# Optimization experiments

Measured on AMD Instinct MI355X. Metric: run time of the kernel, lower is better.

## Reference

```python
import jax, jax.numpy as jnp
import numpy as np

B, T, V, E, H = 128, 256, 50000, 256, 512
H2 = H // 2
NTAGS = 76
START_IDX, STOP_IDX = 74, 75
NEG = -10000.0


def setup_inputs() -> dict:
    key = jax.random.key(0)
    ks = jax.random.split(key, 16)
    input_ids = jax.random.randint(ks[0], (B, T), 0, V, dtype=jnp.int32)
    embed_table = jax.random.normal(ks[1], (V, E), dtype=jnp.float32) * 0.02
    s = 0.05
    Wih_f = jax.random.normal(ks[2], (4 * H2, E)) * s
    Whh_f = jax.random.normal(ks[3], (4 * H2, H2)) * s
    bih_f = jnp.zeros((4 * H2,), jnp.float32)
    bhh_f = jnp.zeros((4 * H2,), jnp.float32)
    Wih_b = jax.random.normal(ks[4], (4 * H2, E)) * s
    Whh_b = jax.random.normal(ks[5], (4 * H2, H2)) * s
    bih_b = jnp.zeros((4 * H2,), jnp.float32)
    bhh_b = jnp.zeros((4 * H2,), jnp.float32)
    # init_hidden uses torch.randn each call -> random initial states
    h0 = jax.random.normal(ks[6], (2, B, H2), dtype=jnp.float32)
    c0 = jax.random.normal(ks[7], (2, B, H2), dtype=jnp.float32)
    W_out = jax.random.normal(ks[8], (NTAGS, H)) * s
    b_out = jnp.zeros((NTAGS,), jnp.float32)
    transitions = jax.random.normal(ks[9], (NTAGS, NTAGS), dtype=jnp.float32)
    transitions = transitions.at[START_IDX, :].set(NEG).at[:, STOP_IDX].set(NEG)
    return dict(input_ids=input_ids, embed_table=embed_table,
                Wih_f=Wih_f, Whh_f=Whh_f, bih_f=bih_f, bhh_f=bhh_f,
                Wih_b=Wih_b, Whh_b=Whh_b, bih_b=bih_b, bhh_b=bhh_b,
                h0=h0, c0=c0, W_out=W_out, b_out=b_out, transitions=transitions)


def _lstm(x, h0, c0, Wih, Whh, bih, bhh):
    # x: [B,T,E] -> outputs [B,T,H2]; PyTorch gate order i,f,g,o
    def step(carry, xt):
        h, c = carry
        gates = xt @ Wih.T + h @ Whh.T + (bih + bhh)  # [B,4*H2]
        i, f, g, o = jnp.split(gates, 4, axis=-1)
        c = jax.nn.sigmoid(f) * c + jax.nn.sigmoid(i) * jnp.tanh(g)
        h = jax.nn.sigmoid(o) * jnp.tanh(c)
        return (h, c), h
    _, hs = jax.lax.scan(step, (h0, c0), jnp.swapaxes(x, 0, 1))  # [T,B,H2]
    return jnp.swapaxes(hs, 0, 1)


def _viterbi(feats, transitions):
    # feats: [T,NTAGS]; transitions[next, prev]
    init = jnp.full((NTAGS,), NEG, feats.dtype).at[START_IDX].set(0.0)

    def step(fv, feat):
        scores = fv[None, :] + transitions          # [next, prev]
        bptr = jnp.argmax(scores, axis=1)           # [NTAGS]
        fv_new = jnp.max(scores, axis=1) + feat
        return fv_new, bptr

    fv, bptrs = jax.lax.scan(step, init, feats)     # bptrs: [T,NTAGS]
    terminal = fv + transitions[STOP_IDX]
    best = jnp.argmax(terminal)
    score = terminal[best]

    def back(tag, bptr):
        return bptr[tag], tag
    _, path = jax.lax.scan(back, best, bptrs, reverse=True)  # [T]
    return score, path


def reference(input_ids, embed_table, Wih_f, Whh_f, bih_f, bhh_f,
              Wih_b, Whh_b, bih_b, bhh_b, h0, c0, W_out, b_out, transitions):
    embeds = embed_table[input_ids]                              # [B,T,E]
    out_f = _lstm(embeds, h0[0], c0[0], Wih_f, Whh_f, bih_f, bhh_f)
    out_b = _lstm(embeds[:, ::-1], h0[1], c0[1], Wih_b, Whh_b, bih_b, bhh_b)[:, ::-1]
    lstm_out = jnp.concatenate([out_f, out_b], axis=-1)          # [B,T,H]
    feats = lstm_out @ W_out.T + b_out                           # [B,T,NTAGS]
    score, path = jax.vmap(_viterbi, in_axes=(0, None))(feats, transitions)
    return score, path
```

## Files before the change

### kernel.cpp

```cpp
#include <hip/hip_runtime.h>
#include <hip/hip_bf16.h>
#include <stdint.h>


#define T_      256
#define NT_     76
#define K3_     768
#define START_  74
#define STOP_   75
#define NEGV    (-10000.0f)

#define OFF_A3    ((size_t)0)
#define OFF_B3T   (OFF_A3    + (size_t)50331648)
#define OFF_XPROJ (OFF_B3T   + (size_t)3145728)
#define OFF_LSTM  (OFF_XPROJ + (size_t)67108864)
#define OFF_HBUF  (OFF_LSTM  + (size_t)67108864)
#define OFF_CBUF  (OFF_HBUF  + (size_t)524288)
#define OFF_CNT   (OFF_CBUF  + (size_t)262144)
#define OFF_FEATS OFF_A3

typedef __attribute__((ext_vector_type(8))) short short8;
typedef __attribute__((ext_vector_type(4))) float float4v;
typedef const __attribute__((address_space(1))) unsigned int gas_uint;
typedef __attribute__((address_space(3))) unsigned int las_uint;

__device__ __forceinline__ unsigned short f2bf(float x) {
    unsigned int u = __float_as_uint(x);
    u = (u + 0x7fffu + ((u >> 16) & 1u)) >> 16;
    return (unsigned short)u;
}
__device__ __forceinline__ float bf2f(unsigned short h) {
    return __uint_as_float(((unsigned int)h) << 16);
}
__device__ __forceinline__ void gl_lds16(const void* g, void* l) {
    __builtin_amdgcn_global_load_lds((gas_uint*)g, (las_uint*)l, 16, 0, 0);
}
__device__ __forceinline__ float4v llc_ld4(const float* p) {
    float4v r;
    asm volatile("global_load_dwordx4 %0, %1, off sc0 sc1" : "=v"(r) : "v"(p) : "memory");
    return r;
}
__device__ __forceinline__ void llc_st(float* p, float v) {
    asm volatile("global_store_dword %0, %1, off sc0 sc1" :: "v"(p), "v"(v) : "memory");
}
__device__ __forceinline__ void wait_vm0() { asm volatile("s_waitcnt vmcnt(0)" ::: "memory"); }

__global__ __launch_bounds__(64) void init_cnt(unsigned int* cnt) {
    if (threadIdx.x < 16) cnt[threadIdx.x * 64] = 0u;
}

__global__ __launch_bounds__(256) void build_a3(const int* __restrict__ ids,
                                                const float* __restrict__ emb,
                                                unsigned short* __restrict__ a3) {
    int m = blockIdx.x, k = threadIdx.x;
    int id = ids[m];
    float x = emb[(size_t)id * 256 + k];
    unsigned short hu = f2bf(x);
    unsigned short lu = f2bf(x - bf2f(hu));
    size_t base = (size_t)m * K3_;
    a3[base + k]       = hu;
    a3[base + 256 + k] = hu;
    a3[base + 512 + k] = lu;
}

__global__ __launch_bounds__(256) void build_b3t(const float* __restrict__ wf,
                                                 const float* __restrict__ wb,
                                                 unsigned short* __restrict__ b3t) {
    int n = blockIdx.x, k = threadIdx.x;
    const float* w = (n < 1024) ? wf : wb;
    int j = n & 1023;
    float x = w[(size_t)j * 256 + k];
    unsigned short hu = f2bf(x);
    unsigned short lu = f2bf(x - bf2f(hu));
    size_t base = (size_t)n * K3_;
    b3t[base + k]       = hu;
    b3t[base + 256 + k] = lu;
    b3t[base + 512 + k] = hu;
}

__global__ __launch_bounds__(256) void gemm_chunk(const unsigned short* __restrict__ A,
                                                  const unsigned short* __restrict__ Bt,
                                                  float* __restrict__ C, int t0) {
    __shared__ __align__(16) unsigned short As[128 * 64];
    __shared__ __align__(16) unsigned short Bs[128 * 64];
    int tid = threadIdx.x, bx = blockIdx.x;
    int d = bx >> 9, rem = bx & 511;
    int tm = rem >> 3, tn = rem & 7;
    int m0 = tm * 128, n0l = tn * 128;
    int tbase = d ? (192 - t0) : t0;
    int lane = tid & 63, wave = tid >> 6;
    int wm = (wave & 1) * 64, wn = (wave >> 1) * 64;
    int quad = lane >> 4, r16 = lane & 15;

    float4v acc[4][4];
#pragma unroll
    for (int i = 0; i < 4; i++)
#pragma unroll
        for (int j = 0; j < 4; j++) acc[i][j] = (float4v){0.f, 0.f, 0.f, 0.f};

    for (int kt = 0; kt < 12; ++kt) {
        int k0 = kt * 64;
#pragma unroll
        for (int i = 0; i < 4; ++i) {
            int c = i * 256 + tid;
            int row = c >> 3, col = c & 7;
            int rowm = m0 + row;
            int arow = (rowm >> 6) * 256 + tbase + (rowm & 63);
            int brow = d * 1024 + n0l + row;
            gl_lds16(A  + (size_t)arow * K3_ + k0 + col * 8, (unsigned short*)As + (size_t)c * 8);
            gl_lds16(Bt + (size_t)brow * K3_ + k0 + col * 8, (unsigned short*)Bs + (size_t)c * 8);
        }
        __syncthreads();
#pragma unroll
        for (int kk = 0; kk < 64; kk += 32) {
            short8 a[4], b[4];
#pragma unroll
            for (int i = 0; i < 4; i++) {
                a[i] = *(const short8*)&As[(wm + i * 16 + r16) * 64 + kk + quad * 8];
                b[i] = *(const short8*)&Bs[(wn + i * 16 + r16) * 64 + kk + quad * 8];
            }
#pragma unroll
            for (int i = 0; i < 4; i++)
#pragma unroll
                for (int j = 0; j < 4; j++)
                    acc[i][j] = __builtin_amdgcn_mfma_f32_16x16x32_bf16(a[i], b[j], acc[i][j], 0, 0, 0);
        }
        __syncthreads();
    }
#pragma unroll
    for (int i = 0; i < 4; i++)
#pragma unroll
        for (int j = 0; j < 4; j++)
#pragma unroll
            for (int r = 0; r < 4; r++) {
                int ml = wm + i * 16 + quad * 4 + r;
                int rowm = m0 + ml;
                int b = rowm >> 6, tl = rowm & 63;
                int n = n0l + wn + j * 16 + r16;
                C[(((size_t)(d * 128 + b)) * 64 + tl) * 1024 + n] = acc[i][j][r];
            }
}

#define HSTR 20

__global__ __launch_bounds__(256) void lstm_rec(
    const float* __restrict__ xproj,
    const float* __restrict__ whh_f, const float* __restrict__ whh_b,
    const float* __restrict__ bih_f, const float* __restrict__ bhh_f,
    const float* __restrict__ bih_b, const float* __restrict__ bhh_b,
    const float* __restrict__ h0,    const float* __restrict__ c0,
    float* __restrict__ lstm_out, float* hbuf, float* cbuf,
    unsigned char* cntbase, int t0) {

    int bx = blockIdx.x;
    int xcd = bx & 7, m8 = bx >> 3;
    int cid = xcd * 2 + (m8 >> 4);
    int s   = m8 & 15;
    int d   = cid & 1, g = cid >> 1;
    int tid = threadIdx.x;

    int q = tid >> 6, r = tid & 63;
    int rowB = (r >> 4) * 256 + s * 16 + (r & 15);
    const float* whh = d ? whh_b : whh_f;
    float4 w4[16];
    {
        const float4* wp = (const float4*)(whh + (size_t)rowB * 256 + q * 64);
#pragma unroll
        for (int i = 0; i < 16; i++) w4[i] = wp[i];
    }

    int b2 = tid >> 4, u2 = tid & 15;
    int ug2 = s * 16 + u2;
    int bg2 = g * 16 + b2;
    const float* bih = d ? bih_b : bih_f;
    const float* bhh = d ? bhh_b : bhh_f;
    float bias[4];
#pragma unroll
    for (int gg = 0; gg < 4; gg++) bias[gg] = bih[gg * 256 + ug2] + bhh[gg * 256 + ug2];
    size_t cidx = ((size_t)d * 128 + bg2) * 256 + ug2;
    float cst = (t0 == 0) ? c0[cidx] : cbuf[cidx];

    __shared__ __align__(16) float h_lds[256 * HSTR];
    __shared__ __align__(16) float red[4 * 64 * HSTR];

    unsigned int* mycnt = (unsigned int*)(cntbase + (size_t)cid * 256);
    const size_t HB_PAR = (size_t)16 * 4096;
    size_t hb_c = (size_t)cid * 4096;

    float xp[4];
    {
        int tloc0 = d ? 63 : 0;
        const float* xb = xproj + (((size_t)(d * 128 + bg2)) * 64 + tloc0) * 1024 + ug2;
#pragma unroll
        for (int gg = 0; gg < 4; gg++) xp[gg] = xb[gg * 256];
    }

    for (int tl = 0; tl < 64; ++tl) {
        int t = t0 + tl;
        int t_src = d ? (255 - t) : t;

        if (t == 0) {
#pragma unroll
            for (int b = 0; b < 16; b++)
                h_lds[tid * HSTR + b] = h0[((size_t)d * 128 + g * 16 + b) * 256 + tid];
        } else {
            const float* hsrc = hbuf + (size_t)(t & 1) * HB_PAR + hb_c + (size_t)tid * 16;
            float4v v0 = llc_ld4(hsrc);
            float4v v1 = llc_ld4(hsrc + 4);
            float4v v2 = llc_ld4(hsrc + 8);
            float4v v3 = llc_ld4(hsrc + 12);
            wait_vm0();
            float4v* dst = (float4v*)&h_lds[tid * HSTR];
            dst[0] = v0; dst[1] = v1; dst[2] = v2; dst[3] = v3;
        }
        __syncthreads();

        float acc[16];
#pragma unroll
        for (int b = 0; b < 16; b++) acc[b] = 0.f;
        const float* hq = h_lds + q * 64 * HSTR;
#pragma unroll
        for (int k4 = 0; k4 < 16; ++k4) {
            float4 wv = w4[k4];
#pragma unroll
            for (int kk = 0; kk < 4; ++kk) {
                float wx = (kk == 0) ? wv.x : (kk == 1) ? wv.y : (kk == 2) ? wv.z : wv.w;
                const float4* hv = (const float4*)(hq + (k4 * 4 + kk) * HSTR);
                float4 ha = hv[0], hb4 = hv[1], hc = hv[2], hd = hv[3];
                acc[0]  += wx * ha.x;  acc[1]  += wx * ha.y;  acc[2]  += wx * ha.z;  acc[3]  += wx * ha.w;
                acc[4]  += wx * hb4.x; acc[5]  += wx * hb4.y; acc[6]  += wx * hb4.z; acc[7]  += wx * hb4.w;
                acc[8]  += wx * hc.x;  acc[9]  += wx * hc.y;  acc[10] += wx * hc.z;  acc[11] += wx * hc.w;
                acc[12] += wx * hd.x;  acc[13] += wx * hd.y;  acc[14] += wx * hd.z;  acc[15] += wx * hd.w;
            }
        }
        {
            float4* rp = (float4*)&red[(q * 64 + r) * HSTR];
            rp[0] = make_float4(acc[0], acc[1], acc[2], acc[3]);
            rp[1] = make_float4(acc[4], acc[5], acc[6], acc[7]);
            rp[2] = make_float4(acc[8], acc[9], acc[10], acc[11]);
            rp[3] = make_float4(acc[12], acc[13], acc[14], acc[15]);
        }
        __syncthreads();

        float gate[4];
#pragma unroll
        for (int gg = 0; gg < 4; gg++) {
            int rr = gg * 16 + u2;
            gate[gg] = red[(0 * 64 + rr) * HSTR + b2] + red[(1 * 64 + rr) * HSTR + b2] +
                       red[(2 * 64 + rr) * HSTR + b2] + red[(3 * 64 + rr) * HSTR + b2] +
                       xp[gg] + bias[gg];
        }
        float iv = 1.f / (1.f + expf(-gate[0]));
        float fv = 1.f / (1.f + expf(-gate[1]));
        float gv = tanhf(gate[2]);
        float ov = 1.f / (1.f + expf(-gate[3]));
        cst = fv * cst + iv * gv;
        float hv = ov * tanhf(cst);

        llc_st(hbuf + (size_t)((t + 1) & 1) * HB_PAR + hb_c + (size_t)ug2 * 16 + b2, hv);
        lstm_out[((size_t)bg2 * 256 + t_src) * 512 + d * 256 + ug2] = hv;
        wait_vm0();

        {
            int tln  = (tl < 63) ? tl + 1 : 63;
            int tloc = d ? (63 - tln) : tln;
            const float* xb = xproj + (((size_t)(d * 128 + bg2)) * 64 + tloc) * 1024 + ug2;
#pragma unroll
            for (int gg = 0; gg < 4; gg++) xp[gg] = xb[gg * 256];
        }
        __builtin_amdgcn_s_barrier();

        if (t < 255) {
            if (tid == 0) {
                __hip_atomic_fetch_add(mycnt, 1u, __ATOMIC_RELAXED, __HIP_MEMORY_SCOPE_AGENT);
                unsigned tgt = 16u * (unsigned)(t + 1);
                while (__hip_atomic_load(mycnt, __ATOMIC_RELAXED, __HIP_MEMORY_SCOPE_AGENT) < tgt)
                    __builtin_amdgcn_s_sleep(1);
            }
            __builtin_amdgcn_s_barrier();
        }
    }
    cbuf[cidx] = cst;
}

__global__ __launch_bounds__(256) void out_proj(const float* __restrict__ lstm,
                                                const float* __restrict__ wout,
                                                const float* __restrict__ bout,
                                                float* __restrict__ feats) {
    __shared__ __align__(16) float hrow[16 * 512];
    int tid = threadIdx.x;
    size_t m0 = (size_t)blockIdx.x * 16;
    {
        const float4* src = (const float4*)(lstm + m0 * 512);
        float4* dst = (float4*)hrow;
        for (int i = tid; i < 2048; i += 256) dst[i] = src[i];
    }
    __syncthreads();
    int n = tid & 127, rh = tid >> 7;
    int nn = (n < NT_) ? n : 0;
    float acc[8];
#pragma unroll
    for (int rr = 0; rr < 8; rr++) acc[rr] = 0.f;
    const float* wrow = wout + (size_t)nn * 512;
    for (int k = 0; k < 512; k += 4) {
        float4 wv = *(const float4*)&wrow[k];
#pragma unroll
        for (int rr = 0; rr < 8; ++rr) {
            float4 hv = *(const float4*)&hrow[(rh * 8 + rr) * 512 + k];
            acc[rr] += wv.x * hv.x + wv.y * hv.y + wv.z * hv.z + wv.w * hv.w;
        }
    }
    if (n < NT_) {
        float bb = bout[n];
#pragma unroll
        for (int rr = 0; rr < 8; ++rr)
            feats[(m0 + rh * 8 + rr) * NT_ + n] = acc[rr] + bb;
    }
}

__global__ __launch_bounds__(128) void viterbi(const float* __restrict__ feats,
                                               const float* __restrict__ trans,
                                               float* __restrict__ out) {
    int b = blockIdx.x, tid = threadIdx.x;
    __shared__ float fvbuf[2][80];
    __shared__ float termbuf[80];
    __shared__ unsigned char bptr[256][NT_];

    float trr[NT_];
    if (tid < NT_) {
#pragma unroll
        for (int p = 0; p < NT_; p++) trr[p] = trans[tid * NT_ + p];
    }
    if (tid < 80) fvbuf[0][tid] = (tid == START_) ? 0.f : NEGV;
    __syncthreads();

    const float* fb = feats + (size_t)b * T_ * NT_;
    for (int t = 0; t < T_; ++t) {
        int par = t & 1;
        if (tid < NT_) {
            float feat = fb[t * NT_ + tid];
            const float* fv = fvbuf[par];
            float best = fv[0] + trr[0];
            int arg = 0;
#pragma unroll
            for (int p = 1; p < NT_; ++p) {
                float sc = fv[p] + trr[p];
                if (sc > best) { best = sc; arg = p; }
            }
            bptr[t][tid] = (unsigned char)arg;
            fvbuf[1 - par][tid] = best + feat;
        }
        __syncthreads();
    }
    if (tid < NT_) termbuf[tid] = fvbuf[0][tid] + trans[STOP_ * NT_ + tid];
    __syncthreads();
    if (tid == 0) {
        float best = termbuf[0];
        int arg = 0;
        for (int p = 1; p < NT_; ++p)
            if (termbuf[p] > best) { best = termbuf[p]; arg = p; }
        out[b] = best;
        int tag = arg;
        float* pout = out + 128 + (size_t)b * T_;
        for (int t = T_ - 1; t >= 0; --t) {
            pout[t] = (float)tag;
            tag = bptr[t][tag];
        }
    }
}

extern "C" void kernel_launch(void* const* d_in, const int* in_sizes, int n_in,
                              void* d_out, int out_size, void* d_ws, size_t ws_size,
                              hipStream_t stream) {
    const int*   ids   = (const int*)  d_in[0];
    const float* emb   = (const float*)d_in[1];
    const float* wih_f = (const float*)d_in[2];
    const float* whh_f = (const float*)d_in[3];
    const float* bih_f = (const float*)d_in[4];
    const float* bhh_f = (const float*)d_in[5];
    const float* wih_b = (const float*)d_in[6];
    const float* whh_b = (const float*)d_in[7];
    const float* bih_b = (const float*)d_in[8];
    const float* bhh_b = (const float*)d_in[9];
    const float* h0    = (const float*)d_in[10];
    const float* c0    = (const float*)d_in[11];
    const float* wout  = (const float*)d_in[12];
    const float* bout  = (const float*)d_in[13];
    const float* trans = (const float*)d_in[14];

    char* ws = (char*)d_ws;
    unsigned short* A3  = (unsigned short*)(ws + OFF_A3);
    unsigned short* B3T = (unsigned short*)(ws + OFF_B3T);
    float* XPROJ        = (float*)(ws + OFF_XPROJ);
    float* LSTM         = (float*)(ws + OFF_LSTM);
    float* HBUF         = (float*)(ws + OFF_HBUF);
    float* CBUF         = (float*)(ws + OFF_CBUF);
    unsigned char* CNT  = (unsigned char*)(ws + OFF_CNT);
    float* FEATS        = (float*)(ws + OFF_FEATS);

    init_cnt <<<1,     64,  0, stream>>>((unsigned int*)CNT);
    build_a3 <<<32768, 256, 0, stream>>>(ids, emb, A3);
    build_b3t<<<2048,  256, 0, stream>>>(wih_f, wih_b, B3T);
    for (int c = 0; c < 4; ++c) {
        gemm_chunk<<<1024, 256, 0, stream>>>(A3, B3T, XPROJ, c * 64);
        lstm_rec  <<<256,  256, 0, stream>>>(XPROJ, whh_f, whh_b, bih_f, bhh_f, bih_b, bhh_b,
                                             h0, c0, LSTM, HBUF, CBUF, CNT, c * 64);
    }
    out_proj<<<2048, 256, 0, stream>>>(LSTM, wout, bout, FEATS);
    viterbi <<<128,  128, 0, stream>>>(FEATS, trans, (float*)d_out);
}
```

Baseline: 2.099 ms.

## Replace atomic counter barrier with step-tagged h exchange in LSTM recurrence

Drops the per-step atomic counter spin barrier between cooperating blocks. Each hidden value is now stored as a 64-bit pair of value and step tag, and readers poll their h slice until every tag matches the current step. The lstm_out writes move to the reader side, and the xproj loads move to the start of each step. This removes the serial atomic and barrier round trips from the critical path, but the h buffer is larger and the polling loads repeat until the data is ready. The tag scheme depends on stale tags from earlier runs never matching the current step.

```diff
diff --git a/kernel.cpp b/kernel.cpp
--- a/kernel.cpp
+++ b/kernel.cpp
@@ -15,12 +15,13 @@
 #define OFF_XPROJ (OFF_B3T   + (size_t)3145728)
 #define OFF_LSTM  (OFF_XPROJ + (size_t)67108864)
 #define OFF_HBUF  (OFF_LSTM  + (size_t)67108864)
-#define OFF_CBUF  (OFF_HBUF  + (size_t)524288)
-#define OFF_CNT   (OFF_CBUF  + (size_t)262144)
+#define OFF_CBUF  (OFF_HBUF  + (size_t)2097152)
 #define OFF_FEATS OFF_A3
 
 typedef __attribute__((ext_vector_type(8))) short short8;
 typedef __attribute__((ext_vector_type(4))) float float4v;
+typedef __attribute__((ext_vector_type(4))) unsigned int uint4v;
+typedef __attribute__((ext_vector_type(2))) unsigned int uint2v;
 typedef const __attribute__((address_space(1))) unsigned int gas_uint;
 typedef __attribute__((address_space(3))) unsigned int las_uint;
 
@@ -35,18 +36,17 @@
 __device__ __forceinline__ void gl_lds16(const void* g, void* l) {
     __builtin_amdgcn_global_load_lds((gas_uint*)g, (las_uint*)l, 16, 0, 0);
 }
-__device__ __forceinline__ float4v llc_ld4(const float* p) {
-    float4v r;
+__device__ __forceinline__ uint4v llc_ld4u(const void* p) {
+    uint4v r;
     asm volatile("global_load_dwordx4 %0, %1, off sc0 sc1" : "=v"(r) : "v"(p) : "memory");
     return r;
 }
-__device__ __forceinline__ void llc_st(float* p, float v) {
-    asm volatile("global_store_dword %0, %1, off sc0 sc1" :: "v"(p), "v"(v) : "memory");
+__device__ __forceinline__ void llc_st2(void* p, uint2v v) {
+    asm volatile("global_store_dwordx2 %0, %1, off sc0 sc1" :: "v"(p), "v"(v) : "memory");
 }
 __device__ __forceinline__ void wait_vm0() { asm volatile("s_waitcnt vmcnt(0)" ::: "memory"); }
-
-__global__ __launch_bounds__(64) void init_cnt(unsigned int* cnt) {
-    if (threadIdx.x < 16) cnt[threadIdx.x * 64] = 0u;
+__device__ __forceinline__ void bar_lgkm() {
+    asm volatile("s_waitcnt lgkmcnt(0)\ns_barrier" ::: "memory");
 }
 
 __global__ __launch_bounds__(256) void build_a3(const int* __restrict__ ids,
@@ -149,8 +149,7 @@
     const float* __restrict__ bih_f, const float* __restrict__ bhh_f,
     const float* __restrict__ bih_b, const float* __restrict__ bhh_b,
     const float* __restrict__ h0,    const float* __restrict__ c0,
-    float* __restrict__ lstm_out, float* hbuf, float* cbuf,
-    unsigned char* cntbase, int t0) {
+    float* __restrict__ lstm_out, unsigned long long* hb, float* cbuf, int t0) {
 
     int bx = blockIdx.x;
     int xcd = bx & 7, m8 = bx >> 3;
@@ -169,7 +168,7 @@
         for (int i = 0; i < 16; i++) w4[i] = wp[i];
     }
 
-    int b2 = tid >> 4, u2 = tid & 15;
+    int u2 = tid >> 4, b2 = tid & 15;
     int ug2 = s * 16 + u2;
     int bg2 = g * 16 + b2;
     const float* bih = d ? bih_b : bih_f;
@@ -181,39 +180,63 @@
     float cst = (t0 == 0) ? c0[cidx] : cbuf[cidx];
 
     __shared__ __align__(16) float h_lds[256 * HSTR];
-    __shared__ __align__(16) float red[4 * 64 * HSTR];
-
-    unsigned int* mycnt = (unsigned int*)(cntbase + (size_t)cid * 256);
+    __shared__ __align__(16) float red[256 * HSTR];
+
     const size_t HB_PAR = (size_t)16 * 4096;
-    size_t hb_c = (size_t)cid * 4096;
-
-    float xp[4];
-    {
-        int tloc0 = d ? 63 : 0;
-        const float* xb = xproj + (((size_t)(d * 128 + bg2)) * 64 + tloc0) * 1024 + ug2;
-#pragma unroll
-        for (int gg = 0; gg < 4; gg++) xp[gg] = xb[gg * 256];
-    }
+    const unsigned long long* hb_rd = hb + (size_t)cid * 4096 + (size_t)tid * 16;
+    unsigned long long* hb_wr = hb + (size_t)cid * 4096 + (size_t)ug2 * 16 + b2;
 
     for (int tl = 0; tl < 64; ++tl) {
         int t = t0 + tl;
-        int t_src = d ? (255 - t) : t;
-
+        int tloc = d ? (63 - tl) : tl;
+
+        float xp[4];
+        {
+            const float* xb = xproj + (((size_t)(d * 128 + bg2)) * 64 + tloc) * 1024 + ug2;
+#pragma unroll
+            for (int gg = 0; gg < 4; gg++) xp[gg] = xb[gg * 256];
+        }
+
+        float4 f[4];
         if (t == 0) {
 #pragma unroll
-            for (int b = 0; b < 16; b++)
-                h_lds[tid * HSTR + b] = h0[((size_t)d * 128 + g * 16 + b) * 256 + tid];
+            for (int i = 0; i < 4; i++)
+#pragma unroll
+                for (int j = 0; j < 4; j++)
+                    ((float*)&f[i])[j] = h0[((size_t)d * 128 + g * 16 + (i * 4 + j)) * 256 + tid];
         } else {
-            const float* hsrc = hbuf + (size_t)(t & 1) * HB_PAR + hb_c + (size_t)tid * 16;
-            float4v v0 = llc_ld4(hsrc);
-            float4v v1 = llc_ld4(hsrc + 4);
-            float4v v2 = llc_ld4(hsrc + 8);
-            float4v v3 = llc_ld4(hsrc + 12);
-            wait_vm0();
-            float4v* dst = (float4v*)&h_lds[tid * HSTR];
-            dst[0] = v0; dst[1] = v1; dst[2] = v2; dst[3] = v3;
-        }
-        __syncthreads();
+            const unsigned long long* src = hb_rd + (size_t)(t & 1) * HB_PAR;
+            unsigned tag = (unsigned)t;
+            uint4v qq[8];
+            for (;;) {
+#pragma unroll
+                for (int i = 0; i < 8; i++) qq[i] = llc_ld4u(src + i * 2);
+                wait_vm0();
+                bool ok = true;
+#pragma unroll
+                for (int i = 0; i < 8; i++) ok &= (qq[i].y == tag) & (qq[i].w == tag);
+                if (ok) break;
+                __builtin_amdgcn_s_sleep(1);
+            }
+            if (tl > 0) {
+                int tsp = d ? (255 - (t - 1)) : (t - 1);
+#pragma unroll
+                for (int b = 0; b < 16; b++) {
+                    unsigned uv = (b & 1) ? qq[b >> 1].z : qq[b >> 1].x;
+                    lstm_out[((size_t)(g * 16 + b) * 256 + tsp) * 512 + d * 256 + tid] =
+                        __uint_as_float(uv);
+                }
+            }
+#pragma unroll
+            for (int i = 0; i < 4; i++)
+                f[i] = make_float4(__uint_as_float(qq[2 * i].x), __uint_as_float(qq[2 * i].z),
+                                   __uint_as_float(qq[2 * i + 1].x), __uint_as_float(qq[2 * i + 1].z));
+        }
+        {
+            float4* dst = (float4*)&h_lds[tid * HSTR];
+            dst[0] = f[0]; dst[1] = f[1]; dst[2] = f[2]; dst[3] = f[3];
+        }
+        bar_lgkm();
 
         float acc[16];
 #pragma unroll
@@ -240,7 +263,7 @@
             rp[2] = make_float4(acc[8], acc[9], acc[10], acc[11]);
             rp[3] = make_float4(acc[12], acc[13], acc[14], acc[15]);
         }
-        __syncthreads();
+        bar_lgkm();
 
         float gate[4];
 #pragma unroll
@@ -257,27 +280,33 @@
         cst = fv * cst + iv * gv;
         float hv = ov * tanhf(cst);
 
-        llc_st(hbuf + (size_t)((t + 1) & 1) * HB_PAR + hb_c + (size_t)ug2 * 16 + b2, hv);
-        lstm_out[((size_t)bg2 * 256 + t_src) * 512 + d * 256 + ug2] = hv;
-        wait_vm0();
-
-        {
-            int tln  = (tl < 63) ? tl + 1 : 63;
-            int tloc = d ? (63 - tln) : tln;
-            const float* xb = xproj + (((size_t)(d * 128 + bg2)) * 64 + tloc) * 1024 + ug2;
-#pragma unroll
-            for (int gg = 0; gg < 4; gg++) xp[gg] = xb[gg * 256];
-        }
-        __builtin_amdgcn_s_barrier();
-
-        if (t < 255) {
-            if (tid == 0) {
-                __hip_atomic_fetch_add(mycnt, 1u, __ATOMIC_RELAXED, __HIP_MEMORY_SCOPE_AGENT);
-                unsigned tgt = 16u * (unsigned)(t + 1);
-                while (__hip_atomic_load(mycnt, __ATOMIC_RELAXED, __HIP_MEMORY_SCOPE_AGENT) < tgt)
-                    __builtin_amdgcn_s_sleep(1);
-            }
-            __builtin_amdgcn_s_barrier();
+        uint2v pk;
+        pk.x = __float_as_uint(hv);
+        pk.y = (unsigned)(t + 1);
+        llc_st2(hb_wr + (size_t)((t + 1) & 1) * HB_PAR, pk);
+    }
+
+    {
+        int te = t0 + 64;
+        const unsigned long long* src = hb_rd + (size_t)(te & 1) * HB_PAR;
+        unsigned tag = (unsigned)te;
+        uint4v qq[8];
+        for (;;) {
+#pragma unroll
+            for (int i = 0; i < 8; i++) qq[i] = llc_ld4u(src + i * 2);
+            wait_vm0();
+            bool ok = true;
+#pragma unroll
+            for (int i = 0; i < 8; i++) ok &= (qq[i].y == tag) & (qq[i].w == tag);
+            if (ok) break;
+            __builtin_amdgcn_s_sleep(1);
+        }
+        int tsp = d ? (255 - (te - 1)) : (te - 1);
+#pragma unroll
+        for (int b = 0; b < 16; b++) {
+            unsigned uv = (b & 1) ? qq[b >> 1].z : qq[b >> 1].x;
+            lstm_out[((size_t)(g * 16 + b) * 256 + tsp) * 512 + d * 256 + tid] =
+                __uint_as_float(uv);
         }
     }
     cbuf[cidx] = cst;
@@ -393,18 +422,16 @@
     unsigned short* B3T = (unsigned short*)(ws + OFF_B3T);
     float* XPROJ        = (float*)(ws + OFF_XPROJ);
     float* LSTM         = (float*)(ws + OFF_LSTM);
-    float* HBUF         = (float*)(ws + OFF_HBUF);
+    unsigned long long* HBUF = (unsigned long long*)(ws + OFF_HBUF);
     float* CBUF         = (float*)(ws + OFF_CBUF);
-    unsigned char* CNT  = (unsigned char*)(ws + OFF_CNT);
     float* FEATS        = (float*)(ws + OFF_FEATS);
 
-    init_cnt <<<1,     64,  0, stream>>>((unsigned int*)CNT);
     build_a3 <<<32768, 256, 0, stream>>>(ids, emb, A3);
     build_b3t<<<2048,  256, 0, stream>>>(wih_f, wih_b, B3T);
     for (int c = 0; c < 4; ++c) {
         gemm_chunk<<<1024, 256, 0, stream>>>(A3, B3T, XPROJ, c * 64);
         lstm_rec  <<<256,  256, 0, stream>>>(XPROJ, whh_f, whh_b, bih_f, bhh_f, bih_b, bhh_b,
-                                             h0, c0, LSTM, HBUF, CBUF, CNT, c * 64);
+                                             h0, c0, LSTM, HBUF, CBUF, c * 64);
     }
     out_proj<<<2048, 256, 0, stream>>>(LSTM, wout, bout, FEATS);
     viterbi <<<128,  128, 0, stream>>>(FEATS, trans, (float*)d_out);
```

Measured after the change: 2.875 ms. +37.0%, slower.
